# Kernel optimization log

Measured on AMD Instinct MI355X. Metric: run time of the kernel, lower is better.

Reference implementation:

```python
import jax, jax.numpy as jnp
import numpy as np

EMBD_SIZE = 128
NUM_HEADS = 8
HEAD_SIZE = 16

def setup_inputs() -> dict:
    key = jax.random.key(0)
    ks = jax.random.split(key, 6)
    B, S = 8, 2048
    x = jax.random.normal(ks[0], (B, S, EMBD_SIZE), dtype=jnp.float32)
    # per-head Linear weights, torch layout [out, in] stacked over heads -> [H, hs, E]
    sc = 1.0 / np.sqrt(EMBD_SIZE)
    Wk = jax.random.normal(ks[1], (NUM_HEADS, HEAD_SIZE, EMBD_SIZE), dtype=jnp.float32) * sc
    Wq = jax.random.normal(ks[2], (NUM_HEADS, HEAD_SIZE, EMBD_SIZE), dtype=jnp.float32) * sc
    Wv = jax.random.normal(ks[3], (NUM_HEADS, HEAD_SIZE, EMBD_SIZE), dtype=jnp.float32) * sc
    Wp = jax.random.normal(ks[4], (EMBD_SIZE, NUM_HEADS * HEAD_SIZE), dtype=jnp.float32) * sc
    bp = jax.random.normal(ks[5], (EMBD_SIZE,), dtype=jnp.float32) * 0.01
    return {"x": x, "Wk": Wk, "Wq": Wq, "Wv": Wv, "Wp": Wp, "bp": bp}

def reference(x, Wk, Wq, Wv, Wp, bp):
    # x: [B,S,E]; W{k,q,v}: [H,hs,E]; Wp: [E,H*hs]
    B, S, E = x.shape
    H, hs, _ = Wk.shape
    q = jnp.einsum('bse,hde->bhsd', x, Wq)
    k = jnp.einsum('bse,hde->bhsd', x, Wk)
    v = jnp.einsum('bse,hde->bhsd', x, Wv)
    # NOTE: original code MULTIPLIES by sqrt(head_size) (k.shape[-1]**0.5)
    scores = jnp.einsum('bhsd,bhtd->bhst', q, k) * (hs ** 0.5)
    wei = jax.nn.softmax(scores, axis=-1)  # dropout is identity in eval mode
    out = jnp.einsum('bhst,bhtd->bhsd', wei, v)
    # concat heads along last dim: [B,S,H*hs]
    out = out.transpose(0, 2, 1, 3).reshape(B, S, H * hs)
    return out @ Wp.T + bp
```

## Files before the change

### kernel.cpp

```cpp
#include <hip/hip_runtime.h>
#include <hip/hip_bf16.h>

constexpr int Bb  = 8;
constexpr int Ss  = 2048;
constexpr int Ee  = 128;
constexpr int Hh  = 8;
constexpr int HSs = 16;
constexpr int QKVSZ = Bb * Hh * Ss * HSs;

typedef _Float16 f16;
typedef __attribute__((ext_vector_type(8)))  _Float16 f16x8;
typedef __attribute__((ext_vector_type(16))) float f32x16;

constexpr float QSCALE = 5.770780163555854f;

__device__ __forceinline__ unsigned pack_rtz(float lo, float hi) {
    union { __fp16 __attribute__((ext_vector_type(2))) h; unsigned u; } c;
    c.h = __builtin_amdgcn_cvt_pkrtz(lo, hi);
    return c.u;
}
__device__ __forceinline__ unsigned pack_rne(float lo, float hi) {
    union { __attribute__((ext_vector_type(2))) _Float16 h; unsigned u; } c;
    c.h[0] = (f16)lo; c.h[1] = (f16)hi;
    return c.u;
}

__device__ __forceinline__ float vmax16(const f32x16& v) {
    float a = fmaxf(fmaxf(v[0],  v[1]),  v[2]);
    float b = fmaxf(fmaxf(v[3],  v[4]),  v[5]);
    float c = fmaxf(fmaxf(v[6],  v[7]),  v[8]);
    float d = fmaxf(fmaxf(v[9],  v[10]), v[11]);
    float e = fmaxf(fmaxf(v[12], v[13]), v[14]);
    float g = fmaxf(fmaxf(a, b), c);
    float h = fmaxf(fmaxf(d, e), v[15]);
    return fmaxf(g, h);
}

__global__ __launch_bounds__(256) void prep_w(
    const float* __restrict__ Wq, const float* __restrict__ Wk,
    const float* __restrict__ Wv, const float* __restrict__ Wp,
    f16* __restrict__ wh)
{
    int i = (blockIdx.x * 256 + threadIdx.x) * 4;
    const float* src = (i < 16384) ? (Wq + i)
                     : (i < 32768) ? (Wk + i - 16384)
                     : (i < 49152) ? (Wv + i - 32768) : (Wp + i - 49152);
    float4 v = *(const float4*)src;
    union { f16 h[4]; uint2 u; } c;
    c.h[0] = (f16)v.x; c.h[1] = (f16)v.y; c.h[2] = (f16)v.z; c.h[3] = (f16)v.w;
    *(uint2*)(wh + i) = c.u;
}

__global__ __launch_bounds__(256) void qkv_kernel(
    const float* __restrict__ x, const f16* __restrict__ wh,
    f16* __restrict__ qo, f16* __restrict__ ko, f16* __restrict__ vo)
{
    constexpr int LDW = 136;
    __shared__ __align__(16) f16 Xs[32 * LDW];

    const int rowbase = blockIdx.x * 32;

    for (int idx = threadIdx.x; idx < 32 * 32; idx += 256) {
        const int r = idx >> 5, cp = idx & 31;
        float4 v = *(const float4*)(x + (size_t)(rowbase + r) * Ee + cp * 4);
        union { f16 h[4]; uint2 u; } cv;
        cv.h[0] = (f16)v.x; cv.h[1] = (f16)v.y; cv.h[2] = (f16)v.z; cv.h[3] = (f16)v.w;
        *(uint2*)&Xs[r * LDW + cp * 4] = cv.u;
    }
    __syncthreads();

    const int wv_ = threadIdx.x >> 6, lane = threadIdx.x & 63;
    const int h = lane >> 5, n31 = lane & 31;

    f16x8 A[8];
#pragma unroll
    for (int t = 0; t < 8; ++t)
        A[t] = *(const f16x8*)&Xs[n31 * LDW + 16 * t + 8 * h];

    const int c = wv_ * 32 + n31;
    const int b = rowbase >> 11;
    const int s0 = rowbase & 2047;
    const int head = c >> 4, d = c & 15;
    const int bh = b * Hh + head;
    const int it = s0 >> 6, g0 = (s0 >> 4) & 3;

#pragma unroll
    for (int mat = 0; mat < 3; ++mat) {
        const f16* wr = wh + mat * 16384 + (size_t)c * Ee + 8 * h;
        f32x16 acc = {};
#pragma unroll
        for (int t = 0; t < 8; ++t)
            acc = __builtin_amdgcn_mfma_f32_32x32x16_f16(A[t], *(const f16x8*)(wr + 16 * t), acc, 0, 0, 0);

        if (mat < 2) {
            f16* dst = (mat == 0) ? qo : ko;
            const float scale = (mat == 1) ? QSCALE : 1.f;
#pragma unroll
            for (int r = 0; r < 16; ++r) {
                const int s = s0 + (r & 3) + 8 * (r >> 2) + 4 * h;
                dst[((size_t)bh * Ss + s) * HSs + d] = (f16)(acc[r] * scale);
            }
        } else {
            f16* vb = vo + (size_t)bh * 65536 + it * 2048;
#pragma unroll
            for (int rq = 0; rq < 4; ++rq) {
                union { f16 hv[4]; uint2 u; } pk4;
#pragma unroll
                for (int i = 0; i < 4; ++i) pk4.hv[i] = (f16)acc[4 * rq + i];
                *(uint2*)(vb + (g0 + (rq >> 1)) * 512 + (d + 32 * h) * 8 + 4 * (rq & 1)) = pk4.u;
            }
        }
    }

    for (int i = threadIdx.x; i < 512; i += 256) {
        const int gp = i >> 8, hd = (i >> 5) & 7, cc = i & 31;
        const int lanep = (cc < 16) ? 16 + cc : 32 + cc;
        const unsigned one2 = 0x3C003C00u;
        uint4 val = ((cc & 15) == 0) ? (uint4){one2, one2, one2, one2}
                                     : (uint4){0, 0, 0, 0};
        *(uint4*)(vo + (size_t)(b * Hh + hd) * 65536 + it * 2048
                  + (g0 + gp) * 512 + lanep * 8) = val;
    }
}

__global__ __launch_bounds__(64, 4) void attn_kernel(
    const f16* __restrict__ qg, const f16* __restrict__ kg,
    const f16* __restrict__ vg, f16* __restrict__ og)
{
    const int blk  = blockIdx.x;
    const int bh   = (blk & 7) * 8 + (blk >> 9);
    const int qblk = (blk >> 3) & 63;
    const int lane = threadIdx.x;
    const int h    = lane >> 5;
    const int q31  = lane & 31;
    const int qbase = qblk * 32;

    const f16x8 qf = *(const f16x8*)(qg + ((size_t)bh * Ss + qbase + q31) * HSs + 8 * h);

    const f16* pk = kg + (size_t)bh * Ss * HSs + q31 * 16 + 8 * h;
    const f16* pv = vg + (size_t)bh * 65536 + lane * 8;

    f16x8 ka0 = *(const f16x8*)pk;
    f16x8 ka1 = *(const f16x8*)(pk + 512);
    f16x8 va0 = *(const f16x8*)(pv);
    f16x8 va1 = *(const f16x8*)(pv + 512);
    f16x8 va2 = *(const f16x8*)(pv + 1024);
    f16x8 va3 = *(const f16x8*)(pv + 1536);

    f32x16 acc = {};
    f32x16 cinit = {};

    constexpr int NIT = Ss / 64;
    for (int it = 0; it < NIT; ++it) {
        f32x16 st0 = __builtin_amdgcn_mfma_f32_32x32x16_f16(ka0, qf, cinit, 0, 0, 0);
        f32x16 st1 = __builtin_amdgcn_mfma_f32_32x32x16_f16(ka1, qf, cinit, 0, 0, 0);

        if (it + 1 < NIT) {
            pk += 1024;
            ka0 = *(const f16x8*)pk;
            ka1 = *(const f16x8*)(pk + 512);
        }

        float mx = fmaxf(vmax16(st0), vmax16(st1));
        mx = fmaxf(mx, __shfl_xor(mx, 32, 64));

        if (__any(mx > 8.f)) {
            const float delta = fmaxf(mx, 0.f);
            const float corr  = __builtin_amdgcn_exp2f(-delta);
#pragma unroll
            for (int r = 0; r < 9; ++r) acc[r] *= corr;
#pragma unroll
            for (int t = 0; t < 16; ++t) { st0[t] -= delta; st1[t] -= delta; }
#pragma unroll
            for (int r = 0; r < 16; ++r) cinit[r] -= delta;
        }

        union { unsigned u[4]; f16x8 v; } B1, B2, B3, B4;
#pragma unroll
        for (int r = 0; r < 4; ++r) {
            B1.u[r] = pack_rtz(__builtin_amdgcn_exp2f(st0[2 * r]),
                               __builtin_amdgcn_exp2f(st0[2 * r + 1]));
            B2.u[r] = pack_rtz(__builtin_amdgcn_exp2f(st0[8 + 2 * r]),
                               __builtin_amdgcn_exp2f(st0[9 + 2 * r]));
            B3.u[r] = pack_rtz(__builtin_amdgcn_exp2f(st1[2 * r]),
                               __builtin_amdgcn_exp2f(st1[2 * r + 1]));
            B4.u[r] = pack_rtz(__builtin_amdgcn_exp2f(st1[8 + 2 * r]),
                               __builtin_amdgcn_exp2f(st1[9 + 2 * r]));
        }

        acc = __builtin_amdgcn_mfma_f32_32x32x16_f16(va0, B1.v, acc, 0, 0, 0);
        acc = __builtin_amdgcn_mfma_f32_32x32x16_f16(va1, B2.v, acc, 0, 0, 0);
        acc = __builtin_amdgcn_mfma_f32_32x32x16_f16(va2, B3.v, acc, 0, 0, 0);
        acc = __builtin_amdgcn_mfma_f32_32x32x16_f16(va3, B4.v, acc, 0, 0, 0);

        if (it + 1 < NIT) {
            pv += 2048;
            va0 = *(const f16x8*)(pv);
            va1 = *(const f16x8*)(pv + 512);
            va2 = *(const f16x8*)(pv + 1024);
            va3 = *(const f16x8*)(pv + 1536);
        }
    }

    const float l = acc[8] + __shfl_xor(acc[8], 32, 64);
    const float inv = 1.f / l;
    const int b = bh >> 3, head = bh & 7;
    f16* op = og + ((size_t)b * Ss + qbase + q31) * Ee + head * HSs;
    uint2 lo = { pack_rne(acc[0] * inv, acc[1] * inv), pack_rne(acc[2] * inv, acc[3] * inv) };
    uint2 hi = { pack_rne(acc[4] * inv, acc[5] * inv), pack_rne(acc[6] * inv, acc[7] * inv) };
    *(uint2*)(op + 4 * h)     = lo;
    *(uint2*)(op + 8 + 4 * h) = hi;
}

__global__ __launch_bounds__(256) void proj_kernel(
    const f16* __restrict__ oh, const f16* __restrict__ wph,
    const float* __restrict__ bp, float* __restrict__ out)
{
    constexpr int LDW = 136;
    __shared__ __align__(16) f16 Os[32 * LDW];
    const int rowbase = blockIdx.x * 32;

    for (int idx = threadIdx.x; idx < 512; idx += 256) {
        const int r = idx >> 4, cp = idx & 15;
        *(f16x8*)&Os[r * LDW + cp * 8] =
            *(const f16x8*)(oh + (size_t)(rowbase + r) * Ee + cp * 8);
    }
    __syncthreads();

    const int wv_ = threadIdx.x >> 6, lane = threadIdx.x & 63;
    const int h = lane >> 5, n31 = lane & 31;

    f16x8 A[8];
#pragma unroll
    for (int t = 0; t < 8; ++t)
        A[t] = *(const f16x8*)&Os[n31 * LDW + 16 * t + 8 * h];

    const int e = wv_ * 32 + n31;
    const f16* wr = wph + (size_t)e * Ee + 8 * h;
    f32x16 acc = {};
#pragma unroll
    for (int t = 0; t < 8; ++t)
        acc = __builtin_amdgcn_mfma_f32_32x32x16_f16(A[t], *(const f16x8*)(wr + 16 * t), acc, 0, 0, 0);

    const float bias = bp[e];
#pragma unroll
    for (int r = 0; r < 16; ++r) {
        const int R = rowbase + (r & 3) + 8 * (r >> 2) + 4 * h;
        out[(size_t)R * Ee + e] = acc[r] + bias;
    }
}

extern "C" void kernel_launch(void* const* d_in, const int* in_sizes, int n_in,
                              void* d_out, int out_size, void* d_ws, size_t ws_size,
                              hipStream_t stream)
{
    const float* x  = (const float*)d_in[0];
    const float* Wk = (const float*)d_in[1];
    const float* Wq = (const float*)d_in[2];
    const float* Wv = (const float*)d_in[3];
    const float* Wp = (const float*)d_in[4];
    const float* bp = (const float*)d_in[5];
    float* out = (float*)d_out;

    f16* ws = (f16*)d_ws;
    f16* qh = ws;
    f16* kh = ws + (size_t)QKVSZ;
    f16* vh = ws + (size_t)2 * QKVSZ;
    f16* oh = ws + (size_t)4 * QKVSZ;
    f16* wh = ws + (size_t)5 * QKVSZ;

    prep_w<<<64, 256, 0, stream>>>(Wq, Wk, Wv, Wp, wh);
    qkv_kernel<<<Bb * Ss / 32, 256, 0, stream>>>(x, wh, qh, kh, vh);
    attn_kernel<<<Bb * Hh * (Ss / 32), 64, 0, stream>>>(qh, kh, vh, oh);
    proj_kernel<<<Bb * Ss / 32, 256, 0, stream>>>(oh, wh + 49152, bp, out);
}
```

Baseline: 134.3 us.

## Fuse output projection into attention kernel and drop weight prep kernel

Attention blocks now hold 8 waves, one per head, for a 32-query tile. Each wave writes its normalized head output into shared memory, and four waves then compute the output projection plus bias directly to the fp32 output. This removes the intermediate fp16 head-output buffer and the separate projection launch. The weight-prep kernel is also removed: the qkv and projection kernels now read fp32 weights and convert them to fp16 in registers, trading extra conversion work and larger weight loads for two fewer launches. Larger blocks with a barrier may change occupancy and scheduling of the attention loop.

New measurement: 133.9 us. No clear change (-0.3%).

```diff
diff --git a/kernel.cpp b/kernel.cpp
--- a/kernel.cpp
+++ b/kernel.cpp
@@ -36,23 +36,17 @@
     return fmaxf(g, h);
 }
 
-__global__ __launch_bounds__(256) void prep_w(
+__device__ __forceinline__ f16x8 cvt8(const float4& w0, const float4& w1) {
+    union { f16x8 v; unsigned u[4]; } wf;
+    wf.u[0] = pack_rne(w0.x, w0.y); wf.u[1] = pack_rne(w0.z, w0.w);
+    wf.u[2] = pack_rne(w1.x, w1.y); wf.u[3] = pack_rne(w1.z, w1.w);
+    return wf.v;
+}
+
+__global__ __launch_bounds__(256) void qkv_kernel(
+    const float* __restrict__ x,
     const float* __restrict__ Wq, const float* __restrict__ Wk,
-    const float* __restrict__ Wv, const float* __restrict__ Wp,
-    f16* __restrict__ wh)
-{
-    int i = (blockIdx.x * 256 + threadIdx.x) * 4;
-    const float* src = (i < 16384) ? (Wq + i)
-                     : (i < 32768) ? (Wk + i - 16384)
-                     : (i < 49152) ? (Wv + i - 32768) : (Wp + i - 49152);
-    float4 v = *(const float4*)src;
-    union { f16 h[4]; uint2 u; } c;
-    c.h[0] = (f16)v.x; c.h[1] = (f16)v.y; c.h[2] = (f16)v.z; c.h[3] = (f16)v.w;
-    *(uint2*)(wh + i) = c.u;
-}
-
-__global__ __launch_bounds__(256) void qkv_kernel(
-    const float* __restrict__ x, const f16* __restrict__ wh,
+    const float* __restrict__ Wv,
     f16* __restrict__ qo, f16* __restrict__ ko, f16* __restrict__ vo)
 {
     constexpr int LDW = 136;
@@ -86,11 +80,15 @@
 
 #pragma unroll
     for (int mat = 0; mat < 3; ++mat) {
-        const f16* wr = wh + mat * 16384 + (size_t)c * Ee + 8 * h;
+        const float* W = (mat == 0) ? Wq : (mat == 1) ? Wk : Wv;
+        const float* wr32 = W + (size_t)c * Ee + 8 * h;
         f32x16 acc = {};
 #pragma unroll
-        for (int t = 0; t < 8; ++t)
-            acc = __builtin_amdgcn_mfma_f32_32x32x16_f16(A[t], *(const f16x8*)(wr + 16 * t), acc, 0, 0, 0);
+        for (int t = 0; t < 8; ++t) {
+            float4 w0 = *(const float4*)(wr32 + 16 * t);
+            float4 w1 = *(const float4*)(wr32 + 16 * t + 4);
+            acc = __builtin_amdgcn_mfma_f32_32x32x16_f16(A[t], cvt8(w0, w1), acc, 0, 0, 0);
+        }
 
         if (mat < 2) {
             f16* dst = (mat == 0) ? qo : ko;
@@ -123,17 +121,22 @@
     }
 }
 
-__global__ __launch_bounds__(64, 4) void attn_kernel(
+__global__ __launch_bounds__(512, 4) void attn_kernel(
     const f16* __restrict__ qg, const f16* __restrict__ kg,
-    const f16* __restrict__ vg, f16* __restrict__ og)
+    const f16* __restrict__ vg, const float* __restrict__ wp32,
+    const float* __restrict__ bp, float* __restrict__ out)
 {
-    const int blk  = blockIdx.x;
-    const int bh   = (blk & 7) * 8 + (blk >> 9);
-    const int qblk = (blk >> 3) & 63;
-    const int lane = threadIdx.x;
+    constexpr int LDW = 136;
+    __shared__ __align__(16) f16 Os[32 * LDW];
+
+    const int b    = blockIdx.x & 7;
+    const int qblk = blockIdx.x >> 3;
+    const int wid  = threadIdx.x >> 6;
+    const int lane = threadIdx.x & 63;
     const int h    = lane >> 5;
     const int q31  = lane & 31;
     const int qbase = qblk * 32;
+    const int bh   = b * Hh + wid;
 
     const f16x8 qf = *(const f16x8*)(qg + ((size_t)bh * Ss + qbase + q31) * HSs + 8 * h);
 
@@ -204,49 +207,36 @@
 
     const float l = acc[8] + __shfl_xor(acc[8], 32, 64);
     const float inv = 1.f / l;
-    const int b = bh >> 3, head = bh & 7;
-    f16* op = og + ((size_t)b * Ss + qbase + q31) * Ee + head * HSs;
+
+    f16* orow = &Os[q31 * LDW + wid * HSs + 4 * h];
     uint2 lo = { pack_rne(acc[0] * inv, acc[1] * inv), pack_rne(acc[2] * inv, acc[3] * inv) };
     uint2 hi = { pack_rne(acc[4] * inv, acc[5] * inv), pack_rne(acc[6] * inv, acc[7] * inv) };
-    *(uint2*)(op + 4 * h)     = lo;
-    *(uint2*)(op + 8 + 4 * h) = hi;
-}
-
-__global__ __launch_bounds__(256) void proj_kernel(
-    const f16* __restrict__ oh, const f16* __restrict__ wph,
-    const float* __restrict__ bp, float* __restrict__ out)
-{
-    constexpr int LDW = 136;
-    __shared__ __align__(16) f16 Os[32 * LDW];
-    const int rowbase = blockIdx.x * 32;
-
-    for (int idx = threadIdx.x; idx < 512; idx += 256) {
-        const int r = idx >> 4, cp = idx & 15;
-        *(f16x8*)&Os[r * LDW + cp * 8] =
-            *(const f16x8*)(oh + (size_t)(rowbase + r) * Ee + cp * 8);
-    }
+    *(uint2*)(orow)     = lo;
+    *(uint2*)(orow + 8) = hi;
     __syncthreads();
 
-    const int wv_ = threadIdx.x >> 6, lane = threadIdx.x & 63;
-    const int h = lane >> 5, n31 = lane & 31;
+    if (wid >= 4) return;
 
     f16x8 A[8];
 #pragma unroll
     for (int t = 0; t < 8; ++t)
-        A[t] = *(const f16x8*)&Os[n31 * LDW + 16 * t + 8 * h];
-
-    const int e = wv_ * 32 + n31;
-    const f16* wr = wph + (size_t)e * Ee + 8 * h;
-    f32x16 acc = {};
-#pragma unroll
-    for (int t = 0; t < 8; ++t)
-        acc = __builtin_amdgcn_mfma_f32_32x32x16_f16(A[t], *(const f16x8*)(wr + 16 * t), acc, 0, 0, 0);
+        A[t] = *(const f16x8*)&Os[q31 * LDW + 16 * t + 8 * h];
+
+    const int e = wid * 32 + q31;
+    const float* wr32 = wp32 + (size_t)e * Ee + 8 * h;
+    f32x16 acc2 = {};
+#pragma unroll
+    for (int t = 0; t < 8; ++t) {
+        float4 w0 = *(const float4*)(wr32 + 16 * t);
+        float4 w1 = *(const float4*)(wr32 + 16 * t + 4);
+        acc2 = __builtin_amdgcn_mfma_f32_32x32x16_f16(A[t], cvt8(w0, w1), acc2, 0, 0, 0);
+    }
 
     const float bias = bp[e];
 #pragma unroll
     for (int r = 0; r < 16; ++r) {
-        const int R = rowbase + (r & 3) + 8 * (r >> 2) + 4 * h;
-        out[(size_t)R * Ee + e] = acc[r] + bias;
+        const int R = qbase + (r & 3) + 8 * (r >> 2) + 4 * h;
+        out[((size_t)b * Ss + R) * Ee + e] = acc2[r] + bias;
     }
 }
 
@@ -266,11 +256,7 @@
     f16* qh = ws;
     f16* kh = ws + (size_t)QKVSZ;
     f16* vh = ws + (size_t)2 * QKVSZ;
-    f16* oh = ws + (size_t)4 * QKVSZ;
-    f16* wh = ws + (size_t)5 * QKVSZ;
-
-    prep_w<<<64, 256, 0, stream>>>(Wq, Wk, Wv, Wp, wh);
-    qkv_kernel<<<Bb * Ss / 32, 256, 0, stream>>>(x, wh, qh, kh, vh);
-    attn_kernel<<<Bb * Hh * (Ss / 32), 64, 0, stream>>>(qh, kh, vh, oh);
-    proj_kernel<<<Bb * Ss / 32, 256, 0, stream>>>(oh, wh + 49152, bp, out);
-}
+
+    qkv_kernel<<<Bb * Ss / 32, 256, 0, stream>>>(x, Wq, Wk, Wv, qh, kh, vh);
+    attn_kernel<<<Bb * Ss / 32, 512, 0, stream>>>(qh, kh, vh, Wp, bp, out);
+}
```
